# Performance work log

Measured on AMD Instinct MI355X. Metric: run time of the kernel, lower is better.

The kernel has to match this reference:

```python
import jax, jax.numpy as jnp
import numpy as np
from jax import lax

B, H, W, C, PS = 2, 192, 192, 96, 8
NWH, NWW = H // PS, W // PS
NW = NWH * NWW  # 576 windows
P2 = PS * PS    # 64


def dwconv3x3(x, w):
    # x: [B, C, H, W], w: [C, 1, 3, 3] depthwise
    return lax.conv_general_dilated(x, w, (1, 1), 'SAME',
                                    dimension_numbers=('NCHW', 'OIHW', 'NCHW'),
                                    feature_group_count=x.shape[1])


def conv1x1(x, w):
    # x: [B, Cin, H, W], w: [Cout, Cin]
    return jnp.einsum('bchw,oc->bohw', x, w)


def patchify(t):
    # t: [B, C, H, W] -> [B*C, nW, ps^2]  (window partition, per-channel tokens)
    t = t.reshape(B, C, NWH, PS, NWW, PS).transpose(0, 1, 2, 4, 3, 5)
    return t.reshape(B * C, NW, P2)


def unpatchify(t):
    # [B*C, nW, ps^2] -> [B, C, H, W]  (window reverse)
    t = t.reshape(B, C, NWH, NWW, PS, PS).transpose(0, 1, 2, 4, 3, 5)
    return t.reshape(B, C, H, W)


def l2norm(t):
    # F.normalize(dim=-1), eps=1e-12
    n = jnp.sqrt(jnp.sum(t * t, axis=-1, keepdims=True))
    return t / jnp.maximum(n, 1e-12)


def setup_inputs() -> dict:
    key = jax.random.key(0)
    ks = jax.random.split(key, 8)
    s = 0.05
    return {
        'x': jax.random.normal(ks[0], (B, H * W, C), jnp.float32),
        'qkv_w': jax.random.normal(ks[1], (3 * C, C), jnp.float32) * s,
        'qkv_dw_w': jax.random.normal(ks[2], (3 * C, 1, 3, 3), jnp.float32) * s,
        'scale': jnp.ones((1, 1, 1), jnp.float32),  # num_heads = 1
        'proj_w': jax.random.normal(ks[3], (C, C), jnp.float32) * s,
        'proj_b': jax.random.normal(ks[4], (C,), jnp.float32) * s,
        'pe_w1': jax.random.normal(ks[5], (C, 1, 3, 3), jnp.float32) * s,
        'pe_w2': jax.random.normal(ks[6], (C, 1, 3, 3), jnp.float32) * s,
    }


def reference(x, qkv_w, qkv_dw_w, scale, proj_w, proj_b, pe_w1, pe_w2):
    xi = x.transpose(0, 2, 1).reshape(B, C, H, W)
    qkv = dwconv3x3(conv1x1(xi, qkv_w), qkv_dw_w)      # [B, 3C, H, W]
    q, k, v_in = jnp.split(qkv, 3, axis=1)             # each [B, C, H, W]

    qp = l2norm(patchify(q))                           # [B*C, nW, ps^2]
    kp = l2norm(patchify(k))
    vp = patchify(v_in)

    logits = jnp.einsum('bnp,bmp->bnm', qp, kp) * scale  # [B*C, nW, nW]
    attn = jax.nn.softmax(logits, axis=-1)
    o = jnp.einsum('bnm,bmp->bnp', attn, vp)             # [B*C, nW, ps^2]

    xo = unpatchify(o)                                   # [B, C, H, W]
    out_c = conv1x1(xo, proj_w) + proj_b[None, :, None, None]
    pe = dwconv3x3(jax.nn.gelu(dwconv3x3(v_in, pe_w1), approximate=False), pe_w2)
    out = out_c + pe                                     # [B, C, H, W]
    return out.reshape(B, C, H * W).transpose(0, 2, 1)   # [B, L, C]
```

## Files before the change

kernel.cpp:

```cpp
#include <hip/hip_runtime.h>
#include <hip/hip_bf16.h>
#include <math.h>

#define BB   2
#define CC   96
#define C3   288
#define HH   192
#define WWI  192
#define HWQ  (HH*WWI)
#define NWH  24
#define NW   576
#define P2   64

typedef float v4f  __attribute__((ext_vector_type(4)));
typedef float f32x4 __attribute__((ext_vector_type(4)));
typedef short s16x8 __attribute__((ext_vector_type(8)));
typedef short s16x4 __attribute__((ext_vector_type(4)));
typedef unsigned short ushort_t;

static __device__ __forceinline__ unsigned short f2bf(float f) {
  __hip_bfloat16 h = __float2bfloat16(f);
  return *reinterpret_cast<unsigned short*>(&h);
}
static __device__ __forceinline__ float bf2f(ushort_t u) {
  union { unsigned u32; float f; } x;
  x.u32 = ((unsigned)u) << 16;
  return x.f;
}

__global__ __launch_bounds__(256) void k0_cvtw(const float* __restrict__ w,
                                               ushort_t* __restrict__ wb, int n) {
  int i = blockIdx.x * 256 + threadIdx.x;
  if (i < n) wb[i] = f2bf(w[i]);
}

__global__ __launch_bounds__(384) void k1_qkv(const float* __restrict__ x,
                                              const ushort_t* __restrict__ qwb,
                                              ushort_t* __restrict__ qkv_bf) {
  __shared__ ushort_t XA[64][104];
  const int tid  = threadIdx.x;
  const int lane = tid & 63;
  const int wv   = tid >> 6;
  const int lq   = lane & 15;
  const int g    = lane >> 4;
  const int m0   = blockIdx.x * 64;
  const int b    = m0 / HWQ;
  const int hwb  = m0 % HWQ;
  const int n0   = wv * 48;

#pragma unroll
  for (int it = 0; it < 4; it++) {
    int idx = tid + it * 384;
    int px = idx / 24, c4 = idx % 24;
    v4f xx = *(const v4f*)(x + (size_t)(m0 + px) * 96 + c4 * 4);
    s16x4 st;
#pragma unroll
    for (int t = 0; t < 4; t++) st[t] = (short)f2bf(xx[t]);
    *(s16x4*)&XA[px][c4 * 4] = st;
  }
  __syncthreads();

  const f32x4 zf = {0.f, 0.f, 0.f, 0.f};
  f32x4 acc[4][3];
#pragma unroll
  for (int mt = 0; mt < 4; mt++)
#pragma unroll
    for (int nt = 0; nt < 3; nt++) acc[mt][nt] = zf;

#pragma unroll
  for (int kk = 0; kk < 3; kk++) {
    s16x8 af[4];
#pragma unroll
    for (int mt = 0; mt < 4; mt++)
      af[mt] = *(const s16x8*)&XA[mt * 16 + lq][kk * 32 + g * 8];
    s16x8 bfr[3];
#pragma unroll
    for (int nt = 0; nt < 3; nt++)
      bfr[nt] = *(const s16x8*)(qwb + (size_t)(n0 + nt * 16 + lq) * 96 + kk * 32 + g * 8);
#pragma unroll
    for (int mt = 0; mt < 4; mt++)
#pragma unroll
      for (int nt = 0; nt < 3; nt++)
        acc[mt][nt] = __builtin_amdgcn_mfma_f32_16x16x32_bf16(af[mt], bfr[nt], acc[mt][nt], 0, 0, 0);
  }

  ushort_t* ob = qkv_bf + (size_t)b * C3 * HWQ;
#pragma unroll
  for (int nt = 0; nt < 3; nt++) {
    int o = n0 + nt * 16 + lq;
#pragma unroll
    for (int mt = 0; mt < 4; mt++) {
      s16x4 st;
#pragma unroll
      for (int t = 0; t < 4; t++) st[t] = (short)f2bf(acc[mt][nt][t]);
      *(s16x4*)(ob + (size_t)o * HWQ + hwb + mt * 16 + g * 4) = st;
    }
  }
}

__global__ __launch_bounds__(256) void k2_dw(const ushort_t* __restrict__ qkv_pre,
                                             const float* __restrict__ dww,
                                             ushort_t* __restrict__ qpo, ushort_t* __restrict__ kpo,
                                             ushort_t* __restrict__ vpo) {
  __shared__ float tin[34][40];
  int bx  = blockIdx.x;
  int b   = bx / (C3 * 36);
  int rem = bx % (C3 * 36);
  int ch  = rem / 36;
  int tile = rem % 36;
  int ty = tile / 6, tx = tile % 6;
  int tid = threadIdx.x;
  const ushort_t* src = qkv_pre + ((size_t)b * C3 + ch) * HWQ;
  const int h0 = ty * 32 - 1, w0 = tx * 32;

  for (int idx = tid; idx < 340; idx += 256) {
    int r = idx / 10, u = idx - r * 10;
    int h = h0 + r;
    bool hok = (h >= 0 && h < HH);
    if (u < 8) {
      v4f f = {0.f, 0.f, 0.f, 0.f};
      if (hok) {
        s16x4 raw = *(const s16x4*)(src + h * WWI + w0 + u * 4);
#pragma unroll
        for (int t = 0; t < 4; t++) f[t] = bf2f((ushort_t)raw[t]);
      }
      *(v4f*)&tin[r][4 + u * 4] = f;
    } else {
      int w = (u == 8) ? (w0 - 1) : (w0 + 32);
      int cdst = (u == 8) ? 3 : 36;
      float f = 0.f;
      if (hok && w >= 0 && w < WWI) f = bf2f(src[h * WWI + w]);
      tin[r][cdst] = f;
    }
  }
  float wv[9];
#pragma unroll
  for (int i = 0; i < 9; i++) wv[i] = dww[ch * 9 + i];
  __syncthreads();

  const int part = ch / CC, c96 = ch % CC;
  const int bc = b * CC + c96;
  const int cc = tid & 31;
  const int s  = tid >> 5;
  const int r0 = 4 * s;

  float a0 = tin[r0][cc + 3],     a1 = tin[r0][cc + 4],     a2 = tin[r0][cc + 5];
  float b0 = tin[r0 + 1][cc + 3], b1 = tin[r0 + 1][cc + 4], b2 = tin[r0 + 1][cc + 5];
  float o[4];
  float ssq = 0.f;
#pragma unroll
  for (int i = 0; i < 4; i++) {
    float c0 = tin[r0 + 2 + i][cc + 3];
    float c1 = tin[r0 + 2 + i][cc + 4];
    float c2 = tin[r0 + 2 + i][cc + 5];
    float acc = wv[0] * a0 + wv[1] * a1 + wv[2] * a2
              + wv[3] * b0 + wv[4] * b1 + wv[5] * b2
              + wv[6] * c0 + wv[7] * c1 + wv[8] * c2;
    o[i] = acc;
    ssq += acc * acc;
    a0 = b0; a1 = b1; a2 = b2;
    b0 = c0; b1 = c1; b2 = c2;
  }

  float inv = 1.f;
  if (part != 2) {
    float t = ssq;
    t += __shfl_xor(t, 1, 64);
    t += __shfl_xor(t, 2, 64);
    t += __shfl_xor(t, 4, 64);
    t += __shfl_xor(t, 32, 64);
    inv = 1.f / fmaxf(sqrtf(t), 1e-12f);
  }

  ushort_t* dst = (part == 0) ? qpo : ((part == 1) ? kpo : vpo);
  int n = (ty * 4 + (s >> 1)) * NWH + tx * 4 + (cc >> 3);
  int prow0 = r0 & 7;
  int pcol  = cc & 7;
  ushort_t* op = dst + ((size_t)bc * NW + n) * P2;
#pragma unroll
  for (int i = 0; i < 4; i++)
    op[(prow0 + i) * 8 + pcol] = f2bf(o[i] * inv);
}

__device__ __forceinline__ void stage_v(const ushort_t* __restrict__ vb,
                                        ushort_t* __restrict__ dst, int tid) {
#pragma unroll
  for (int it = 0; it < 3; it++) {
    int idx = tid + it * 192;
    if (it < 2 || idx < 512) {
      int kv = idx & 63, c = idx >> 6;
      s16x8 v = *(const s16x8*)(vb + kv * 64 + c * 8);
#pragma unroll
      for (int t = 0; t < 8; t++) {
        int p = c * 8 + t;
        dst[p * 64 + (kv ^ ((p & 7) << 3))] = (ushort_t)v[t];
      }
    }
  }
}

__device__ __forceinline__ void stage_k(const ushort_t* __restrict__ kb,
                                        ushort_t* __restrict__ dst, int tid) {
#pragma unroll
  for (int it = 0; it < 3; it++) {
    int idx = tid + it * 192;
    if (it < 2 || idx < 512) {
      int kv = idx >> 3, c = idx & 7;
      s16x8 v = *(const s16x8*)(kb + kv * 64 + c * 8);
      *(s16x8*)&dst[kv * 64 + ((c * 8) ^ ((kv & 7) << 3))] = v;
    }
  }
}

__global__ __launch_bounds__(192, 2) void k3_attn(const ushort_t* __restrict__ qp,
                                                  const ushort_t* __restrict__ kp,
                                                  const ushort_t* __restrict__ vp,
                                                  const float* __restrict__ scale_p,
                                                  ushort_t* __restrict__ o_p) {
  __shared__ ushort_t VT[2][4096];
  __shared__ ushort_t KT[2][4096];
  const int tid  = threadIdx.x;
  const int lane = tid & 63;
  const int wv   = tid >> 6;
  const int lq   = lane & 15;
  const int g    = lane >> 4;
  const int bid  = blockIdx.x;
  const int gw   = (bid & 7) * 144 + (bid >> 3);
  const int bc   = gw / 6;
  const int qch  = gw % 6;
  const int q0   = qch * 96 + wv * 32;
  const float sl = scale_p[0];

  const ushort_t* qpb = qp + (size_t)bc * NW * 64;
  const ushort_t* kpb = kp + (size_t)bc * NW * 64;
  const ushort_t* vpb = vp + (size_t)bc * NW * 64;

  s16x8 qf[2][2];
#pragma unroll
  for (int nt = 0; nt < 2; nt++)
#pragma unroll
    for (int ks = 0; ks < 2; ks++)
      qf[nt][ks] = *(const s16x8*)(qpb + (size_t)(q0 + nt * 16 + lq) * 64 + ks * 32 + g * 8);

  const f32x4 zf = {0.f, 0.f, 0.f, 0.f};
  f32x4 Oa[2][4];
#pragma unroll
  for (int a = 0; a < 2; a++)
#pragma unroll
    for (int b2 = 0; b2 < 4; b2++) Oa[a][b2] = zf;
  float lsum[2] = {0.f, 0.f};

  stage_k(kpb, KT[0], tid);
  stage_v(vpb, VT[0], tid);
  __syncthreads();

  const int s0 = lq + ((lane & 16) << 1);

  for (int kt = 0; kt < 9; kt++) {
    const int cur = kt & 1;
    if (kt < 8) {
      stage_k(kpb + (kt + 1) * 4096, KT[cur ^ 1], tid);
      stage_v(vpb + (kt + 1) * 4096, VT[cur ^ 1], tid);
    }

    f32x4 s[4][2];
#pragma unroll
    for (int a = 0; a < 4; a++)
#pragma unroll
      for (int b2 = 0; b2 < 2; b2++) s[a][b2] = zf;
#pragma unroll
    for (int ks = 0; ks < 2; ks++) {
      s16x8 kf[4];
#pragma unroll
      for (int mt = 0; mt < 4; mt++)
        kf[mt] = *(const s16x8*)&KT[cur][(mt * 16 + lq) * 64 + ((ks * 32 + g * 8) ^ ((lq & 7) << 3))];
#pragma unroll
      for (int mt = 0; mt < 4; mt++)
#pragma unroll
        for (int nt = 0; nt < 2; nt++)
          s[mt][nt] = __builtin_amdgcn_mfma_f32_16x16x32_bf16(kf[mt], qf[nt][ks], s[mt][nt], 0, 0, 0);
    }

    unsigned pk[2][4][2];
#pragma unroll
    for (int nt = 0; nt < 2; nt++) {
      float rs = 0.f;
#pragma unroll
      for (int mt = 0; mt < 4; mt++) {
        float e0 = __expf(s[mt][nt][0] * sl);
        float e1 = __expf(s[mt][nt][1] * sl);
        float e2 = __expf(s[mt][nt][2] * sl);
        float e3 = __expf(s[mt][nt][3] * sl);
        rs += (e0 + e1) + (e2 + e3);
        pk[nt][mt][0] = (unsigned)f2bf(e0) | ((unsigned)f2bf(e1) << 16);
        pk[nt][mt][1] = (unsigned)f2bf(e2) | ((unsigned)f2bf(e3) << 16);
      }
      lsum[nt] += rs;
    }

#pragma unroll
    for (int ks2 = 0; ks2 < 2; ks2++) {
      s16x8 vf[4];
#pragma unroll
      for (int ntd = 0; ntd < 4; ntd++) {
        int p = ntd * 16 + lq;
        vf[ntd] = *(const s16x8*)&VT[cur][p * 64 + ((ks2 * 32 + g * 8) ^ ((p & 7) << 3))];
      }
#pragma unroll
      for (int qt = 0; qt < 2; qt++) {
        union { s16x8 v; unsigned u[4]; } af;
#pragma unroll
        for (int w = 0; w < 4; w++) {
          int src = s0 + ((w >> 1) << 4);
          unsigned lo = __shfl(pk[qt][2 * ks2 + 0][w & 1], src, 64);
          unsigned hi = __shfl(pk[qt][2 * ks2 + 1][w & 1], src, 64);
          af.u[w] = (lane & 32) ? hi : lo;
        }
#pragma unroll
        for (int ntd = 0; ntd < 4; ntd++)
          Oa[qt][ntd] = __builtin_amdgcn_mfma_f32_16x16x32_bf16(af.v, vf[ntd], Oa[qt][ntd], 0, 0, 0);
      }
    }
    __syncthreads();
  }

  float inv[2];
#pragma unroll
  for (int nt = 0; nt < 2; nt++) {
    float v = lsum[nt];
    v += __shfl_xor(v, 16, 64);
    v += __shfl_xor(v, 32, 64);
    inv[nt] = 1.f / v;
  }
  ushort_t* ob = o_p + ((size_t)bc * NW + q0) * 64;
#pragma unroll
  for (int qt = 0; qt < 2; qt++) {
#pragma unroll
    for (int r = 0; r < 4; r++) {
      float iv = __shfl(inv[qt], g * 4 + r, 64);
#pragma unroll
      for (int ntd = 0; ntd < 4; ntd++)
        ob[(qt * 16 + g * 4 + r) * 64 + ntd * 16 + lq] = f2bf(Oa[qt][ntd][r] * iv);
    }
  }
}

__global__ __launch_bounds__(256) void k4_pe(const ushort_t* __restrict__ vp,
                                             const float* __restrict__ w1p,
                                             const float* __restrict__ w2p,
                                             ushort_t* __restrict__ pe) {
  __shared__ float vt[36][38];
  __shared__ float gt[34][36];
  int bx = blockIdx.x;
  int b = bx / (CC * 36);
  int rem = bx % (CC * 36);
  int c = rem / 36;
  int tile = rem % 36;
  int ty = tile / 6, tx = tile % 6;
  int tid = threadIdx.x;
  const ushort_t* src = vp + ((size_t)(b * CC + c)) * NW * P2;
  int h0 = ty * 32 - 2, w0 = tx * 32 - 2;
  for (int idx = tid; idx < 36 * 36; idx += 256) {
    int r = idx / 36, cc2 = idx % 36;
    int h = h0 + r, w = w0 + cc2;
    float v = 0.f;
    if (h >= 0 && h < HH && w >= 0 && w < WWI) {
      int n2 = (h >> 3) * NWH + (w >> 3);
      int p2 = ((h & 7) << 3) | (w & 7);
      v = bf2f(src[(size_t)n2 * P2 + p2]);
    }
    vt[r][cc2] = v;
  }
  __syncthreads();
  float w1[9], w2[9];
#pragma unroll
  for (int i = 0; i < 9; i++) { w1[i] = w1p[c * 9 + i]; w2[i] = w2p[c * 9 + i]; }
  for (int idx = tid; idx < 34 * 34; idx += 256) {
    int r = idx / 34, cc2 = idx % 34;
    int gh = ty * 32 + r - 1, gw = tx * 32 + cc2 - 1;
    float a = 0.f;
#pragma unroll
    for (int dy = 0; dy < 3; dy++)
#pragma unroll
      for (int dx = 0; dx < 3; dx++)
        a += w1[dy * 3 + dx] * vt[r + dy][cc2 + dx];
    float gv = 0.5f * a * (1.f + erff(a * 0.70710678118f));
    gt[r][cc2] = (gh >= 0 && gh < HH && gw >= 0 && gw < WWI) ? gv : 0.f;
  }
  __syncthreads();
  ushort_t* dst = pe + ((size_t)(b * CC + c)) * HWQ;
  for (int idx = tid; idx < 1024; idx += 256) {
    int hl = idx >> 5, wl = idx & 31;
    float a = 0.f;
#pragma unroll
    for (int dy = 0; dy < 3; dy++)
#pragma unroll
      for (int dx = 0; dx < 3; dx++)
        a += w2[dy * 3 + dx] * gt[hl + dy][wl + dx];
    dst[(ty * 32 + hl) * WWI + tx * 32 + wl] = f2bf(a);
  }
}

__global__ __launch_bounds__(384) void k5_proj(const ushort_t* __restrict__ o_p,
                                               const ushort_t* __restrict__ pwb,
                                               const float* __restrict__ pb,
                                               const ushort_t* __restrict__ pe,
                                               float* __restrict__ out) {
  __shared__ ushort_t xo[96][104];
  const int bx = blockIdx.x;
  const int b = bx / NW, n = bx % NW;
  const int wr = n / NWH, wc = n % NWH;
  const int tid = threadIdx.x;
#pragma unroll
  for (int it = 0; it < 2; it++) {
    int idx = tid + it * 384;
    int c = idx >> 3, ch = idx & 7;
    *(s16x8*)&xo[c][ch * 8] =
        *(const s16x8*)(o_p + ((size_t)(b * CC + c) * NW + n) * P2 + ch * 8);
  }
  __syncthreads();
  const int lane = tid & 63, wv = tid >> 6;
  const int lq = lane & 15, g = lane >> 4;
  const int o = wv * 16 + lq;
  s16x8 bfr[3];
#pragma unroll
  for (int kk = 0; kk < 3; kk++)
    bfr[kk] = *(const s16x8*)(pwb + (size_t)o * 96 + kk * 32 + g * 8);
  const f32x4 zf = {0.f, 0.f, 0.f, 0.f};
  f32x4 acc[4] = {zf, zf, zf, zf};
#pragma unroll
  for (int kk = 0; kk < 3; kk++) {
#pragma unroll
    for (int mt = 0; mt < 4; mt++) {
      s16x8 a;
#pragma unroll
      for (int j = 0; j < 8; j++)
        a[j] = (short)xo[kk * 32 + g * 8 + j][mt * 16 + lq];
      acc[mt] = __builtin_amdgcn_mfma_f32_16x16x32_bf16(a, bfr[kk], acc[mt], 0, 0, 0);
    }
  }
  const float pbv = pb[o];
  const ushort_t* per = pe + ((size_t)(b * CC + o)) * HWQ;
  float* ob = out + (size_t)b * HWQ * CC;
#pragma unroll
  for (int mt = 0; mt < 4; mt++) {
    int p = mt * 16 + g * 4;
    int hw = (wr * 8 + (p >> 3)) * WWI + wc * 8 + (p & 7);
    s16x4 pv = *(const s16x4*)(per + hw);
#pragma unroll
    for (int r = 0; r < 4; r++)
      ob[(size_t)(hw + r) * CC + o] = acc[mt][r] + pbv + bf2f((ushort_t)pv[r]);
  }
}

extern "C" void kernel_launch(void* const* d_in, const int* in_sizes, int n_in,
                              void* d_out, int out_size, void* d_ws, size_t ws_size,
                              hipStream_t stream) {
  const float* x        = (const float*)d_in[0];
  const float* qkv_w    = (const float*)d_in[1];
  const float* qkv_dw_w = (const float*)d_in[2];
  const float* scale    = (const float*)d_in[3];
  const float* proj_w   = (const float*)d_in[4];
  const float* proj_b   = (const float*)d_in[5];
  const float* pe_w1    = (const float*)d_in[6];
  const float* pe_w2    = (const float*)d_in[7];
  float* ws = (float*)d_ws;

  ushort_t* qkv_bf = (ushort_t*)ws;
  ushort_t* o_p    = (ushort_t*)ws;
  ushort_t* pe     = (ushort_t*)(ws + 10616832);
  ushort_t* qp     = (ushort_t*)(ws + 17694720);
  ushort_t* kp     = (ushort_t*)(ws + 21233664);
  ushort_t* vp     = (ushort_t*)(ws + 24772608);
  ushort_t* qwb    = (ushort_t*)(ws + 28311552);
  ushort_t* pwb    = (ushort_t*)(ws + 28325376);

  float* out = (float*)d_out;

  hipLaunchKernelGGL(k0_cvtw, dim3(108), dim3(256), 0, stream, qkv_w, qwb, C3 * CC);
  hipLaunchKernelGGL(k0_cvtw, dim3(36), dim3(256), 0, stream, proj_w, pwb, CC * CC);
  hipLaunchKernelGGL(k1_qkv, dim3((BB * HWQ) / 64), dim3(384), 0, stream, x, qwb, qkv_bf);
  hipLaunchKernelGGL(k2_dw, dim3(BB * C3 * 36), dim3(256), 0, stream,
                     qkv_bf, qkv_dw_w, qp, kp, vp);
  hipLaunchKernelGGL(k3_attn, dim3(BB * CC * 6), dim3(192), 0, stream, qp, kp, vp, scale, o_p);
  hipLaunchKernelGGL(k4_pe, dim3(BB * CC * 36), dim3(256), 0, stream, vp, pe_w1, pe_w2, pe);
  hipLaunchKernelGGL(k5_proj, dim3(BB * NW), dim3(384), 0, stream, o_p, pwb, proj_b, pe, out);
}
```

Baseline: 160.5 us.

## Fuse positional-encoding convs into depthwise kernel and merge weight conversions

The V-channel blocks of the depthwise qkv kernel now load a wider halo, recompute the depthwise conv over a 36x36 region, write the V patches, and then run the two pe 3x3 convs with GELU in shared memory. This removes the separate pe kernel and its strided re-read of the patchified V. The two weight-conversion launches are also merged into one. In exchange, V blocks do much more work than Q/K blocks, which causes load imbalance, and every block now reserves about 17 KB of LDS, which may lower occupancy.

```diff
diff --git a/kernel.cpp b/kernel.cpp
--- a/kernel.cpp
+++ b/kernel.cpp
@@ -28,10 +28,14 @@
   return x.f;
 }
 
-__global__ __launch_bounds__(256) void k0_cvtw(const float* __restrict__ w,
-                                               ushort_t* __restrict__ wb, int n) {
+__global__ __launch_bounds__(256) void k0_cvtw2(const float* __restrict__ a,
+                                                ushort_t* __restrict__ ab, int na,
+                                                const float* __restrict__ b,
+                                                ushort_t* __restrict__ bb, int nb) {
   int i = blockIdx.x * 256 + threadIdx.x;
-  if (i < n) wb[i] = f2bf(w[i]);
+  if (i < na) ab[i] = f2bf(a[i]);
+  int j = i - na;
+  if (j >= 0 && j < nb) bb[j] = f2bf(b[j]);
 }
 
 __global__ __launch_bounds__(384) void k1_qkv(const float* __restrict__ x,
@@ -100,9 +104,11 @@
 
 __global__ __launch_bounds__(256) void k2_dw(const ushort_t* __restrict__ qkv_pre,
                                              const float* __restrict__ dww,
+                                             const float* __restrict__ w1p,
+                                             const float* __restrict__ w2p,
                                              ushort_t* __restrict__ qpo, ushort_t* __restrict__ kpo,
-                                             ushort_t* __restrict__ vpo) {
-  __shared__ float tin[34][40];
+                                             ushort_t* __restrict__ vpo, ushort_t* __restrict__ pe) {
+  __shared__ float lds[4336];
   int bx  = blockIdx.x;
   int b   = bx / (C3 * 36);
   int rem = bx % (C3 * 36);
@@ -111,75 +117,156 @@
   int ty = tile / 6, tx = tile % 6;
   int tid = threadIdx.x;
   const ushort_t* src = qkv_pre + ((size_t)b * C3 + ch) * HWQ;
-  const int h0 = ty * 32 - 1, w0 = tx * 32;
-
-  for (int idx = tid; idx < 340; idx += 256) {
-    int r = idx / 10, u = idx - r * 10;
-    int h = h0 + r;
-    bool hok = (h >= 0 && h < HH);
-    if (u < 8) {
-      v4f f = {0.f, 0.f, 0.f, 0.f};
-      if (hok) {
-        s16x4 raw = *(const s16x4*)(src + h * WWI + w0 + u * 4);
-#pragma unroll
-        for (int t = 0; t < 4; t++) f[t] = bf2f((ushort_t)raw[t]);
-      }
-      *(v4f*)&tin[r][4 + u * 4] = f;
-    } else {
-      int w = (u == 8) ? (w0 - 1) : (w0 + 32);
-      int cdst = (u == 8) ? 3 : 36;
-      float f = 0.f;
-      if (hok && w >= 0 && w < WWI) f = bf2f(src[h * WWI + w]);
-      tin[r][cdst] = f;
-    }
-  }
-  float wv[9];
-#pragma unroll
-  for (int i = 0; i < 9; i++) wv[i] = dww[ch * 9 + i];
-  __syncthreads();
-
   const int part = ch / CC, c96 = ch % CC;
   const int bc = b * CC + c96;
-  const int cc = tid & 31;
-  const int s  = tid >> 5;
-  const int r0 = 4 * s;
-
-  float a0 = tin[r0][cc + 3],     a1 = tin[r0][cc + 4],     a2 = tin[r0][cc + 5];
-  float b0 = tin[r0 + 1][cc + 3], b1 = tin[r0 + 1][cc + 4], b2 = tin[r0 + 1][cc + 5];
-  float o[4];
-  float ssq = 0.f;
-#pragma unroll
-  for (int i = 0; i < 4; i++) {
-    float c0 = tin[r0 + 2 + i][cc + 3];
-    float c1 = tin[r0 + 2 + i][cc + 4];
-    float c2 = tin[r0 + 2 + i][cc + 5];
-    float acc = wv[0] * a0 + wv[1] * a1 + wv[2] * a2
-              + wv[3] * b0 + wv[4] * b1 + wv[5] * b2
-              + wv[6] * c0 + wv[7] * c1 + wv[8] * c2;
-    o[i] = acc;
-    ssq += acc * acc;
-    a0 = b0; a1 = b1; a2 = b2;
-    b0 = c0; b1 = c1; b2 = c2;
-  }
-
-  float inv = 1.f;
+  const int w0 = tx * 32;
+  float wv[9];
+#pragma unroll
+  for (int i = 0; i < 9; i++) wv[i] = dww[ch * 9 + i];
+
   if (part != 2) {
+    float* tin = lds;
+    const int h0 = ty * 32 - 1;
+    for (int idx = tid; idx < 340; idx += 256) {
+      int r = idx / 10, u = idx - r * 10;
+      int h = h0 + r;
+      bool hok = (h >= 0 && h < HH);
+      if (u < 8) {
+        v4f f = {0.f, 0.f, 0.f, 0.f};
+        if (hok) {
+          s16x4 raw = *(const s16x4*)(src + h * WWI + w0 + u * 4);
+#pragma unroll
+          for (int t = 0; t < 4; t++) f[t] = bf2f((ushort_t)raw[t]);
+        }
+        *(v4f*)&tin[r * 40 + 4 + u * 4] = f;
+      } else {
+        int w = (u == 8) ? (w0 - 1) : (w0 + 32);
+        int cdst = (u == 8) ? 3 : 36;
+        float f = 0.f;
+        if (hok && w >= 0 && w < WWI) f = bf2f(src[h * WWI + w]);
+        tin[r * 40 + cdst] = f;
+      }
+    }
+    __syncthreads();
+
+    const int cc = tid & 31;
+    const int s  = tid >> 5;
+    const int r0 = 4 * s;
+    float a0 = tin[r0 * 40 + cc + 3],       a1 = tin[r0 * 40 + cc + 4],       a2 = tin[r0 * 40 + cc + 5];
+    float b0 = tin[(r0 + 1) * 40 + cc + 3], b1 = tin[(r0 + 1) * 40 + cc + 4], b2 = tin[(r0 + 1) * 40 + cc + 5];
+    float o[4];
+    float ssq = 0.f;
+#pragma unroll
+    for (int i = 0; i < 4; i++) {
+      float c0 = tin[(r0 + 2 + i) * 40 + cc + 3];
+      float c1 = tin[(r0 + 2 + i) * 40 + cc + 4];
+      float c2 = tin[(r0 + 2 + i) * 40 + cc + 5];
+      float acc = wv[0] * a0 + wv[1] * a1 + wv[2] * a2
+                + wv[3] * b0 + wv[4] * b1 + wv[5] * b2
+                + wv[6] * c0 + wv[7] * c1 + wv[8] * c2;
+      o[i] = acc;
+      ssq += acc * acc;
+      a0 = b0; a1 = b1; a2 = b2;
+      b0 = c0; b1 = c1; b2 = c2;
+    }
     float t = ssq;
     t += __shfl_xor(t, 1, 64);
     t += __shfl_xor(t, 2, 64);
     t += __shfl_xor(t, 4, 64);
     t += __shfl_xor(t, 32, 64);
-    inv = 1.f / fmaxf(sqrtf(t), 1e-12f);
-  }
-
-  ushort_t* dst = (part == 0) ? qpo : ((part == 1) ? kpo : vpo);
-  int n = (ty * 4 + (s >> 1)) * NWH + tx * 4 + (cc >> 3);
-  int prow0 = r0 & 7;
-  int pcol  = cc & 7;
-  ushort_t* op = dst + ((size_t)bc * NW + n) * P2;
-#pragma unroll
-  for (int i = 0; i < 4; i++)
-    op[(prow0 + i) * 8 + pcol] = f2bf(o[i] * inv);
+    float inv = 1.f / fmaxf(sqrtf(t), 1e-12f);
+
+    ushort_t* dst = (part == 0) ? qpo : kpo;
+    int n = (ty * 4 + (s >> 1)) * NWH + tx * 4 + (cc >> 3);
+    int prow0 = r0 & 7;
+    int pcol  = cc & 7;
+    ushort_t* op = dst + ((size_t)bc * NW + n) * P2;
+#pragma unroll
+    for (int i = 0; i < 4; i++)
+      op[(prow0 + i) * 8 + pcol] = f2bf(o[i] * inv);
+  } else {
+    float* tin38 = lds;
+    float* vt    = lds + 1672;
+    float* gt    = lds + 3112;
+    float w1[9], w2[9];
+#pragma unroll
+    for (int i = 0; i < 9; i++) { w1[i] = w1p[c96 * 9 + i]; w2[i] = w2p[c96 * 9 + i]; }
+    const int h0v = ty * 32 - 3;
+    for (int idx = tid; idx < 380; idx += 256) {
+      int r = idx / 10, u = idx - r * 10;
+      int h = h0v + r;
+      bool hok = (h >= 0 && h < HH);
+      if (u < 8) {
+        v4f f = {0.f, 0.f, 0.f, 0.f};
+        if (hok) {
+          s16x4 raw = *(const s16x4*)(src + h * WWI + w0 + u * 4);
+#pragma unroll
+          for (int t = 0; t < 4; t++) f[t] = bf2f((ushort_t)raw[t]);
+        }
+        *(v4f*)&tin38[r * 44 + 4 + u * 4] = f;
+      } else if (u == 8) {
+#pragma unroll
+        for (int t = 0; t < 3; t++) {
+          int w = w0 - 3 + t;
+          float f = 0.f;
+          if (hok && w >= 0) f = bf2f(src[h * WWI + w]);
+          tin38[r * 44 + 1 + t] = f;
+        }
+      } else {
+#pragma unroll
+        for (int t = 0; t < 3; t++) {
+          int w = w0 + 32 + t;
+          float f = 0.f;
+          if (hok && w < WWI) f = bf2f(src[h * WWI + w]);
+          tin38[r * 44 + 36 + t] = f;
+        }
+      }
+    }
+    __syncthreads();
+    for (int idx = tid; idx < 1296; idx += 256) {
+      int rv = idx / 36, cv = idx % 36;
+      int h = ty * 32 - 2 + rv, w = tx * 32 - 2 + cv;
+      float a = 0.f;
+#pragma unroll
+      for (int dy = 0; dy < 3; dy++)
+#pragma unroll
+        for (int dx = 0; dx < 3; dx++)
+          a += wv[dy * 3 + dx] * tin38[(rv + dy) * 44 + cv + 1 + dx];
+      vt[rv * 40 + cv] = (h >= 0 && h < HH && w >= 0 && w < WWI) ? a : 0.f;
+    }
+    __syncthreads();
+    for (int idx = tid; idx < 1024; idx += 256) {
+      int hl = idx >> 5, wl = idx & 31;
+      float v = vt[(hl + 2) * 40 + wl + 2];
+      int n = (ty * 4 + (hl >> 3)) * NWH + tx * 4 + (wl >> 3);
+      int p = ((hl & 7) << 3) | (wl & 7);
+      vpo[((size_t)bc * NW + n) * P2 + p] = f2bf(v);
+    }
+    for (int idx = tid; idx < 1156; idx += 256) {
+      int rg = idx / 34, cg = idx % 34;
+      int gh = ty * 32 - 1 + rg, gw2 = tx * 32 - 1 + cg;
+      float a = 0.f;
+#pragma unroll
+      for (int dy = 0; dy < 3; dy++)
+#pragma unroll
+        for (int dx = 0; dx < 3; dx++)
+          a += w1[dy * 3 + dx] * vt[(rg + dy) * 40 + cg + dx];
+      float gv = 0.5f * a * (1.f + erff(a * 0.70710678118f));
+      gt[rg * 36 + cg] = (gh >= 0 && gh < HH && gw2 >= 0 && gw2 < WWI) ? gv : 0.f;
+    }
+    __syncthreads();
+    ushort_t* dst = pe + ((size_t)bc) * HWQ;
+    for (int idx = tid; idx < 1024; idx += 256) {
+      int hl = idx >> 5, wl = idx & 31;
+      float a = 0.f;
+#pragma unroll
+      for (int dy = 0; dy < 3; dy++)
+#pragma unroll
+        for (int dx = 0; dx < 3; dx++)
+          a += w2[dy * 3 + dx] * gt[(hl + dy) * 36 + wl + dx];
+      dst[(ty * 32 + hl) * WWI + tx * 32 + wl] = f2bf(a);
+    }
+  }
 }
 
 __device__ __forceinline__ void stage_v(const ushort_t* __restrict__ vb,
@@ -345,62 +432,6 @@
   }
 }
 
-__global__ __launch_bounds__(256) void k4_pe(const ushort_t* __restrict__ vp,
-                                             const float* __restrict__ w1p,
-                                             const float* __restrict__ w2p,
-                                             ushort_t* __restrict__ pe) {
-  __shared__ float vt[36][38];
-  __shared__ float gt[34][36];
-  int bx = blockIdx.x;
-  int b = bx / (CC * 36);
-  int rem = bx % (CC * 36);
-  int c = rem / 36;
-  int tile = rem % 36;
-  int ty = tile / 6, tx = tile % 6;
-  int tid = threadIdx.x;
-  const ushort_t* src = vp + ((size_t)(b * CC + c)) * NW * P2;
-  int h0 = ty * 32 - 2, w0 = tx * 32 - 2;
-  for (int idx = tid; idx < 36 * 36; idx += 256) {
-    int r = idx / 36, cc2 = idx % 36;
-    int h = h0 + r, w = w0 + cc2;
-    float v = 0.f;
-    if (h >= 0 && h < HH && w >= 0 && w < WWI) {
-      int n2 = (h >> 3) * NWH + (w >> 3);
-      int p2 = ((h & 7) << 3) | (w & 7);
-      v = bf2f(src[(size_t)n2 * P2 + p2]);
-    }
-    vt[r][cc2] = v;
-  }
-  __syncthreads();
-  float w1[9], w2[9];
-#pragma unroll
-  for (int i = 0; i < 9; i++) { w1[i] = w1p[c * 9 + i]; w2[i] = w2p[c * 9 + i]; }
-  for (int idx = tid; idx < 34 * 34; idx += 256) {
-    int r = idx / 34, cc2 = idx % 34;
-    int gh = ty * 32 + r - 1, gw = tx * 32 + cc2 - 1;
-    float a = 0.f;
-#pragma unroll
-    for (int dy = 0; dy < 3; dy++)
-#pragma unroll
-      for (int dx = 0; dx < 3; dx++)
-        a += w1[dy * 3 + dx] * vt[r + dy][cc2 + dx];
-    float gv = 0.5f * a * (1.f + erff(a * 0.70710678118f));
-    gt[r][cc2] = (gh >= 0 && gh < HH && gw >= 0 && gw < WWI) ? gv : 0.f;
-  }
-  __syncthreads();
-  ushort_t* dst = pe + ((size_t)(b * CC + c)) * HWQ;
-  for (int idx = tid; idx < 1024; idx += 256) {
-    int hl = idx >> 5, wl = idx & 31;
-    float a = 0.f;
-#pragma unroll
-    for (int dy = 0; dy < 3; dy++)
-#pragma unroll
-      for (int dx = 0; dx < 3; dx++)
-        a += w2[dy * 3 + dx] * gt[hl + dy][wl + dx];
-    dst[(ty * 32 + hl) * WWI + tx * 32 + wl] = f2bf(a);
-  }
-}
-
 __global__ __launch_bounds__(384) void k5_proj(const ushort_t* __restrict__ o_p,
                                                const ushort_t* __restrict__ pwb,
                                                const float* __restrict__ pb,
@@ -477,12 +508,11 @@
 
   float* out = (float*)d_out;
 
-  hipLaunchKernelGGL(k0_cvtw, dim3(108), dim3(256), 0, stream, qkv_w, qwb, C3 * CC);
-  hipLaunchKernelGGL(k0_cvtw, dim3(36), dim3(256), 0, stream, proj_w, pwb, CC * CC);
+  hipLaunchKernelGGL(k0_cvtw2, dim3(144), dim3(256), 0, stream,
+                     qkv_w, qwb, C3 * CC, proj_w, pwb, CC * CC);
   hipLaunchKernelGGL(k1_qkv, dim3((BB * HWQ) / 64), dim3(384), 0, stream, x, qwb, qkv_bf);
   hipLaunchKernelGGL(k2_dw, dim3(BB * C3 * 36), dim3(256), 0, stream,
-                     qkv_bf, qkv_dw_w, qp, kp, vp);
+                     qkv_bf, qkv_dw_w, pe_w1, pe_w2, qp, kp, vp, pe);
   hipLaunchKernelGGL(k3_attn, dim3(BB * CC * 6), dim3(192), 0, stream, qp, kp, vp, scale, o_p);
-  hipLaunchKernelGGL(k4_pe, dim3(BB * CC * 36), dim3(256), 0, stream, vp, pe_w1, pe_w2, pe);
   hipLaunchKernelGGL(k5_proj, dim3(BB * NW), dim3(384), 0, stream, o_p, pwb, proj_b, pe, out);
 }
```

Measured after the change: 156.7 us. -2.4%, faster.

## Merge attention and positional-encoding kernels into one launch, fuse weight conversions

Applied to the files above, without the earlier changes.

Combines the attention kernel and the depthwise-conv/GELU positional-encoding kernel into a single launch, where block IDs select which role a block plays and both share one shared-memory buffer. The aim is to let the independent PE blocks run alongside attention blocks, filling idle compute units, and to remove a launch gap. It also merges the two weight-conversion launches into one. PE blocks now run with 192 threads and are bound to the attention kernel's launch bounds, which may reduce their efficiency.

```diff
diff --git a/kernel.cpp b/kernel.cpp
--- a/kernel.cpp
+++ b/kernel.cpp
@@ -28,10 +28,14 @@
   return x.f;
 }
 
-__global__ __launch_bounds__(256) void k0_cvtw(const float* __restrict__ w,
-                                               ushort_t* __restrict__ wb, int n) {
+__global__ __launch_bounds__(256) void k0_cvtw2(const float* __restrict__ a,
+                                                ushort_t* __restrict__ ab, int na,
+                                                const float* __restrict__ b,
+                                                ushort_t* __restrict__ bb, int nb) {
   int i = blockIdx.x * 256 + threadIdx.x;
-  if (i < n) wb[i] = f2bf(w[i]);
+  if (i < na) ab[i] = f2bf(a[i]);
+  int j = i - na;
+  if (j >= 0 && j < nb) bb[j] = f2bf(b[j]);
 }
 
 __global__ __launch_bounds__(384) void k1_qkv(const float* __restrict__ x,
@@ -212,192 +216,195 @@
   }
 }
 
-__global__ __launch_bounds__(192, 2) void k3_attn(const ushort_t* __restrict__ qp,
-                                                  const ushort_t* __restrict__ kp,
-                                                  const ushort_t* __restrict__ vp,
-                                                  const float* __restrict__ scale_p,
-                                                  ushort_t* __restrict__ o_p) {
-  __shared__ ushort_t VT[2][4096];
-  __shared__ ushort_t KT[2][4096];
-  const int tid  = threadIdx.x;
-  const int lane = tid & 63;
-  const int wv   = tid >> 6;
-  const int lq   = lane & 15;
-  const int g    = lane >> 4;
-  const int bid  = blockIdx.x;
-  const int gw   = (bid & 7) * 144 + (bid >> 3);
-  const int bc   = gw / 6;
-  const int qch  = gw % 6;
-  const int q0   = qch * 96 + wv * 32;
-  const float sl = scale_p[0];
-
-  const ushort_t* qpb = qp + (size_t)bc * NW * 64;
-  const ushort_t* kpb = kp + (size_t)bc * NW * 64;
-  const ushort_t* vpb = vp + (size_t)bc * NW * 64;
-
-  s16x8 qf[2][2];
-#pragma unroll
-  for (int nt = 0; nt < 2; nt++)
-#pragma unroll
-    for (int ks = 0; ks < 2; ks++)
-      qf[nt][ks] = *(const s16x8*)(qpb + (size_t)(q0 + nt * 16 + lq) * 64 + ks * 32 + g * 8);
-
-  const f32x4 zf = {0.f, 0.f, 0.f, 0.f};
-  f32x4 Oa[2][4];
-#pragma unroll
-  for (int a = 0; a < 2; a++)
-#pragma unroll
-    for (int b2 = 0; b2 < 4; b2++) Oa[a][b2] = zf;
-  float lsum[2] = {0.f, 0.f};
-
-  stage_k(kpb, KT[0], tid);
-  stage_v(vpb, VT[0], tid);
-  __syncthreads();
-
-  const int s0 = lq + ((lane & 16) << 1);
-
-  for (int kt = 0; kt < 9; kt++) {
-    const int cur = kt & 1;
-    if (kt < 8) {
-      stage_k(kpb + (kt + 1) * 4096, KT[cur ^ 1], tid);
-      stage_v(vpb + (kt + 1) * 4096, VT[cur ^ 1], tid);
-    }
-
-    f32x4 s[4][2];
-#pragma unroll
-    for (int a = 0; a < 4; a++)
-#pragma unroll
-      for (int b2 = 0; b2 < 2; b2++) s[a][b2] = zf;
-#pragma unroll
-    for (int ks = 0; ks < 2; ks++) {
-      s16x8 kf[4];
-#pragma unroll
-      for (int mt = 0; mt < 4; mt++)
-        kf[mt] = *(const s16x8*)&KT[cur][(mt * 16 + lq) * 64 + ((ks * 32 + g * 8) ^ ((lq & 7) << 3))];
-#pragma unroll
-      for (int mt = 0; mt < 4; mt++)
-#pragma unroll
-        for (int nt = 0; nt < 2; nt++)
-          s[mt][nt] = __builtin_amdgcn_mfma_f32_16x16x32_bf16(kf[mt], qf[nt][ks], s[mt][nt], 0, 0, 0);
-    }
-
-    unsigned pk[2][4][2];
+__global__ __launch_bounds__(192, 2) void k3_attn_pe(const ushort_t* __restrict__ qp,
+                                                     const ushort_t* __restrict__ kp,
+                                                     const ushort_t* __restrict__ vp,
+                                                     const float* __restrict__ scale_p,
+                                                     ushort_t* __restrict__ o_p,
+                                                     const float* __restrict__ w1p,
+                                                     const float* __restrict__ w2p,
+                                                     ushort_t* __restrict__ pe) {
+  __shared__ ushort_t SMEM[16384];
+  const int tid = threadIdx.x;
+
+  if (blockIdx.x < BB * CC * 6) {
+    const int lane = tid & 63;
+    const int wv   = tid >> 6;
+    const int lq   = lane & 15;
+    const int g    = lane >> 4;
+    const int bid  = blockIdx.x;
+    const int gw   = (bid & 7) * 144 + (bid >> 3);
+    const int bc   = gw / 6;
+    const int qch  = gw % 6;
+    const int q0   = qch * 96 + wv * 32;
+    const float sl = scale_p[0];
+
+    const ushort_t* qpb = qp + (size_t)bc * NW * 64;
+    const ushort_t* kpb = kp + (size_t)bc * NW * 64;
+    const ushort_t* vpb = vp + (size_t)bc * NW * 64;
+    ushort_t* VT0 = SMEM;
+    ushort_t* KT0 = SMEM + 8192;
+
+    s16x8 qf[2][2];
+#pragma unroll
+    for (int nt = 0; nt < 2; nt++)
+#pragma unroll
+      for (int ks = 0; ks < 2; ks++)
+        qf[nt][ks] = *(const s16x8*)(qpb + (size_t)(q0 + nt * 16 + lq) * 64 + ks * 32 + g * 8);
+
+    const f32x4 zf = {0.f, 0.f, 0.f, 0.f};
+    f32x4 Oa[2][4];
+#pragma unroll
+    for (int a = 0; a < 2; a++)
+#pragma unroll
+      for (int b2 = 0; b2 < 4; b2++) Oa[a][b2] = zf;
+    float lsum[2] = {0.f, 0.f};
+
+    stage_k(kpb, KT0, tid);
+    stage_v(vpb, VT0, tid);
+    __syncthreads();
+
+    const int s0 = lq + ((lane & 16) << 1);
+
+    for (int kt = 0; kt < 9; kt++) {
+      const int cur = kt & 1;
+      ushort_t* VTc = VT0 + cur * 4096;
+      ushort_t* KTc = KT0 + cur * 4096;
+      if (kt < 8) {
+        stage_k(kpb + (kt + 1) * 4096, KT0 + (cur ^ 1) * 4096, tid);
+        stage_v(vpb + (kt + 1) * 4096, VT0 + (cur ^ 1) * 4096, tid);
+      }
+
+      f32x4 s[4][2];
+#pragma unroll
+      for (int a = 0; a < 4; a++)
+#pragma unroll
+        for (int b2 = 0; b2 < 2; b2++) s[a][b2] = zf;
+#pragma unroll
+      for (int ks = 0; ks < 2; ks++) {
+        s16x8 kf[4];
+#pragma unroll
+        for (int mt = 0; mt < 4; mt++)
+          kf[mt] = *(const s16x8*)&KTc[(mt * 16 + lq) * 64 + ((ks * 32 + g * 8) ^ ((lq & 7) << 3))];
+#pragma unroll
+        for (int mt = 0; mt < 4; mt++)
+#pragma unroll
+          for (int nt = 0; nt < 2; nt++)
+            s[mt][nt] = __builtin_amdgcn_mfma_f32_16x16x32_bf16(kf[mt], qf[nt][ks], s[mt][nt], 0, 0, 0);
+      }
+
+      unsigned pk[2][4][2];
+#pragma unroll
+      for (int nt = 0; nt < 2; nt++) {
+        float rs = 0.f;
+#pragma unroll
+        for (int mt = 0; mt < 4; mt++) {
+          float e0 = __expf(s[mt][nt][0] * sl);
+          float e1 = __expf(s[mt][nt][1] * sl);
+          float e2 = __expf(s[mt][nt][2] * sl);
+          float e3 = __expf(s[mt][nt][3] * sl);
+          rs += (e0 + e1) + (e2 + e3);
+          pk[nt][mt][0] = (unsigned)f2bf(e0) | ((unsigned)f2bf(e1) << 16);
+          pk[nt][mt][1] = (unsigned)f2bf(e2) | ((unsigned)f2bf(e3) << 16);
+        }
+        lsum[nt] += rs;
+      }
+
+#pragma unroll
+      for (int ks2 = 0; ks2 < 2; ks2++) {
+        s16x8 vf[4];
+#pragma unroll
+        for (int ntd = 0; ntd < 4; ntd++) {
+          int p = ntd * 16 + lq;
+          vf[ntd] = *(const s16x8*)&VTc[p * 64 + ((ks2 * 32 + g * 8) ^ ((p & 7) << 3))];
+        }
+#pragma unroll
+        for (int qt = 0; qt < 2; qt++) {
+          union { s16x8 v; unsigned u[4]; } af;
+#pragma unroll
+          for (int w = 0; w < 4; w++) {
+            int src = s0 + ((w >> 1) << 4);
+            unsigned lo = __shfl(pk[qt][2 * ks2 + 0][w & 1], src, 64);
+            unsigned hi = __shfl(pk[qt][2 * ks2 + 1][w & 1], src, 64);
+            af.u[w] = (lane & 32) ? hi : lo;
+          }
+#pragma unroll
+          for (int ntd = 0; ntd < 4; ntd++)
+            Oa[qt][ntd] = __builtin_amdgcn_mfma_f32_16x16x32_bf16(af.v, vf[ntd], Oa[qt][ntd], 0, 0, 0);
+        }
+      }
+      __syncthreads();
+    }
+
+    float inv[2];
 #pragma unroll
     for (int nt = 0; nt < 2; nt++) {
-      float rs = 0.f;
-#pragma unroll
-      for (int mt = 0; mt < 4; mt++) {
-        float e0 = __expf(s[mt][nt][0] * sl);
-        float e1 = __expf(s[mt][nt][1] * sl);
-        float e2 = __expf(s[mt][nt][2] * sl);
-        float e3 = __expf(s[mt][nt][3] * sl);
-        rs += (e0 + e1) + (e2 + e3);
-        pk[nt][mt][0] = (unsigned)f2bf(e0) | ((unsigned)f2bf(e1) << 16);
-        pk[nt][mt][1] = (unsigned)f2bf(e2) | ((unsigned)f2bf(e3) << 16);
-      }
-      lsum[nt] += rs;
-    }
-
-#pragma unroll
-    for (int ks2 = 0; ks2 < 2; ks2++) {
-      s16x8 vf[4];
-#pragma unroll
-      for (int ntd = 0; ntd < 4; ntd++) {
-        int p = ntd * 16 + lq;
-        vf[ntd] = *(const s16x8*)&VT[cur][p * 64 + ((ks2 * 32 + g * 8) ^ ((p & 7) << 3))];
-      }
-#pragma unroll
-      for (int qt = 0; qt < 2; qt++) {
-        union { s16x8 v; unsigned u[4]; } af;
-#pragma unroll
-        for (int w = 0; w < 4; w++) {
-          int src = s0 + ((w >> 1) << 4);
-          unsigned lo = __shfl(pk[qt][2 * ks2 + 0][w & 1], src, 64);
-          unsigned hi = __shfl(pk[qt][2 * ks2 + 1][w & 1], src, 64);
-          af.u[w] = (lane & 32) ? hi : lo;
-        }
+      float v = lsum[nt];
+      v += __shfl_xor(v, 16, 64);
+      v += __shfl_xor(v, 32, 64);
+      inv[nt] = 1.f / v;
+    }
+    ushort_t* ob = o_p + ((size_t)bc * NW + q0) * 64;
+#pragma unroll
+    for (int qt = 0; qt < 2; qt++) {
+#pragma unroll
+      for (int r = 0; r < 4; r++) {
+        float iv = __shfl(inv[qt], g * 4 + r, 64);
 #pragma unroll
         for (int ntd = 0; ntd < 4; ntd++)
-          Oa[qt][ntd] = __builtin_amdgcn_mfma_f32_16x16x32_bf16(af.v, vf[ntd], Oa[qt][ntd], 0, 0, 0);
-      }
-    }
+          ob[(qt * 16 + g * 4 + r) * 64 + ntd * 16 + lq] = f2bf(Oa[qt][ntd][r] * iv);
+      }
+    }
+  } else {
+    float* vt = (float*)SMEM;
+    float* gt = ((float*)SMEM) + 1368;
+    int pid = blockIdx.x - BB * CC * 6;
+    int b = pid / (CC * 36);
+    int rem = pid % (CC * 36);
+    int c = rem / 36;
+    int tile = rem % 36;
+    int ty = tile / 6, tx = tile % 6;
+    const ushort_t* src = vp + ((size_t)(b * CC + c)) * NW * P2;
+    int h0 = ty * 32 - 2, w0 = tx * 32 - 2;
+    for (int idx = tid; idx < 36 * 36; idx += 192) {
+      int r = idx / 36, cc2 = idx % 36;
+      int h = h0 + r, w = w0 + cc2;
+      float v = 0.f;
+      if (h >= 0 && h < HH && w >= 0 && w < WWI) {
+        int n2 = (h >> 3) * NWH + (w >> 3);
+        int p2 = ((h & 7) << 3) | (w & 7);
+        v = bf2f(src[(size_t)n2 * P2 + p2]);
+      }
+      vt[r * 38 + cc2] = v;
+    }
+    float w1[9], w2[9];
+#pragma unroll
+    for (int i = 0; i < 9; i++) { w1[i] = w1p[c * 9 + i]; w2[i] = w2p[c * 9 + i]; }
     __syncthreads();
-  }
-
-  float inv[2];
-#pragma unroll
-  for (int nt = 0; nt < 2; nt++) {
-    float v = lsum[nt];
-    v += __shfl_xor(v, 16, 64);
-    v += __shfl_xor(v, 32, 64);
-    inv[nt] = 1.f / v;
-  }
-  ushort_t* ob = o_p + ((size_t)bc * NW + q0) * 64;
-#pragma unroll
-  for (int qt = 0; qt < 2; qt++) {
-#pragma unroll
-    for (int r = 0; r < 4; r++) {
-      float iv = __shfl(inv[qt], g * 4 + r, 64);
-#pragma unroll
-      for (int ntd = 0; ntd < 4; ntd++)
-        ob[(qt * 16 + g * 4 + r) * 64 + ntd * 16 + lq] = f2bf(Oa[qt][ntd][r] * iv);
-    }
-  }
-}
-
-__global__ __launch_bounds__(256) void k4_pe(const ushort_t* __restrict__ vp,
-                                             const float* __restrict__ w1p,
-                                             const float* __restrict__ w2p,
-                                             ushort_t* __restrict__ pe) {
-  __shared__ float vt[36][38];
-  __shared__ float gt[34][36];
-  int bx = blockIdx.x;
-  int b = bx / (CC * 36);
-  int rem = bx % (CC * 36);
-  int c = rem / 36;
-  int tile = rem % 36;
-  int ty = tile / 6, tx = tile % 6;
-  int tid = threadIdx.x;
-  const ushort_t* src = vp + ((size_t)(b * CC + c)) * NW * P2;
-  int h0 = ty * 32 - 2, w0 = tx * 32 - 2;
-  for (int idx = tid; idx < 36 * 36; idx += 256) {
-    int r = idx / 36, cc2 = idx % 36;
-    int h = h0 + r, w = w0 + cc2;
-    float v = 0.f;
-    if (h >= 0 && h < HH && w >= 0 && w < WWI) {
-      int n2 = (h >> 3) * NWH + (w >> 3);
-      int p2 = ((h & 7) << 3) | (w & 7);
-      v = bf2f(src[(size_t)n2 * P2 + p2]);
-    }
-    vt[r][cc2] = v;
-  }
-  __syncthreads();
-  float w1[9], w2[9];
-#pragma unroll
-  for (int i = 0; i < 9; i++) { w1[i] = w1p[c * 9 + i]; w2[i] = w2p[c * 9 + i]; }
-  for (int idx = tid; idx < 34 * 34; idx += 256) {
-    int r = idx / 34, cc2 = idx % 34;
-    int gh = ty * 32 + r - 1, gw = tx * 32 + cc2 - 1;
-    float a = 0.f;
-#pragma unroll
-    for (int dy = 0; dy < 3; dy++)
-#pragma unroll
-      for (int dx = 0; dx < 3; dx++)
-        a += w1[dy * 3 + dx] * vt[r + dy][cc2 + dx];
-    float gv = 0.5f * a * (1.f + erff(a * 0.70710678118f));
-    gt[r][cc2] = (gh >= 0 && gh < HH && gw >= 0 && gw < WWI) ? gv : 0.f;
-  }
-  __syncthreads();
-  ushort_t* dst = pe + ((size_t)(b * CC + c)) * HWQ;
-  for (int idx = tid; idx < 1024; idx += 256) {
-    int hl = idx >> 5, wl = idx & 31;
-    float a = 0.f;
-#pragma unroll
-    for (int dy = 0; dy < 3; dy++)
-#pragma unroll
-      for (int dx = 0; dx < 3; dx++)
-        a += w2[dy * 3 + dx] * gt[hl + dy][wl + dx];
-    dst[(ty * 32 + hl) * WWI + tx * 32 + wl] = f2bf(a);
+    for (int idx = tid; idx < 34 * 34; idx += 192) {
+      int r = idx / 34, cc2 = idx % 34;
+      int gh = ty * 32 + r - 1, gw2 = tx * 32 + cc2 - 1;
+      float a = 0.f;
+#pragma unroll
+      for (int dy = 0; dy < 3; dy++)
+#pragma unroll
+        for (int dx = 0; dx < 3; dx++)
+          a += w1[dy * 3 + dx] * vt[(r + dy) * 38 + cc2 + dx];
+      float gv = 0.5f * a * (1.f + erff(a * 0.70710678118f));
+      gt[r * 36 + cc2] = (gh >= 0 && gh < HH && gw2 >= 0 && gw2 < WWI) ? gv : 0.f;
+    }
+    __syncthreads();
+    ushort_t* dst = pe + ((size_t)(b * CC + c)) * HWQ;
+    for (int idx = tid; idx < 1024; idx += 192) {
+      int hl = idx >> 5, wl = idx & 31;
+      float a = 0.f;
+#pragma unroll
+      for (int dy = 0; dy < 3; dy++)
+#pragma unroll
+        for (int dx = 0; dx < 3; dx++)
+          a += w2[dy * 3 + dx] * gt[(hl + dy) * 36 + wl + dx];
+      dst[(ty * 32 + hl) * WWI + tx * 32 + wl] = f2bf(a);
+    }
   }
 }
 
@@ -477,12 +484,12 @@
 
   float* out = (float*)d_out;
 
-  hipLaunchKernelGGL(k0_cvtw, dim3(108), dim3(256), 0, stream, qkv_w, qwb, C3 * CC);
-  hipLaunchKernelGGL(k0_cvtw, dim3(36), dim3(256), 0, stream, proj_w, pwb, CC * CC);
+  hipLaunchKernelGGL(k0_cvtw2, dim3(144), dim3(256), 0, stream,
+                     qkv_w, qwb, C3 * CC, proj_w, pwb, CC * CC);
   hipLaunchKernelGGL(k1_qkv, dim3((BB * HWQ) / 64), dim3(384), 0, stream, x, qwb, qkv_bf);
   hipLaunchKernelGGL(k2_dw, dim3(BB * C3 * 36), dim3(256), 0, stream,
                      qkv_bf, qkv_dw_w, qp, kp, vp);
-  hipLaunchKernelGGL(k3_attn, dim3(BB * CC * 6), dim3(192), 0, stream, qp, kp, vp, scale, o_p);
-  hipLaunchKernelGGL(k4_pe, dim3(BB * CC * 36), dim3(256), 0, stream, vp, pe_w1, pe_w2, pe);
+  hipLaunchKernelGGL(k3_attn_pe, dim3(BB * CC * 6 + BB * CC * 36), dim3(192), 0, stream,
+                     qp, kp, vp, scale, o_p, pe_w1, pe_w2, pe);
   hipLaunchKernelGGL(k5_proj, dim3(BB * NW), dim3(384), 0, stream, o_p, pwb, proj_b, pe, out);
 }
```

After: 158.8 us. No clear change (-1.1%).
